# Performance work log

Measured on AMD Instinct MI355X. Metric: run time of the kernel, lower is better.

The kernel has to match this reference:

```python
import jax, jax.numpy as jnp
import numpy as np

B, S, D = 2, 2048, 2048
H, KVH, HD = 16, 8, 128
EPS = 1e-6
ROPE_THETA = 10000.0


def _rope_cache(seq_len, head_dim):
    inv_freq = 1.0 / (ROPE_THETA ** (np.arange(0, head_dim, 2, dtype=np.float32) / head_dim))
    t = np.arange(seq_len, dtype=np.float32)
    freqs = np.outer(t, inv_freq)                      # [S, HD/2]
    emb = np.concatenate([freqs, freqs], axis=-1)      # [S, HD]
    return jnp.asarray(np.cos(emb)), jnp.asarray(np.sin(emb))


def setup_inputs() -> dict:
    key = jax.random.key(0)
    ks = jax.random.split(key, 10)
    x = jax.random.normal(ks[0], (B, S, D), dtype=jnp.float32)
    wq_q = jax.random.randint(ks[1], (H * HD, D), -127, 128, dtype=jnp.int32)
    wk_q = jax.random.randint(ks[2], (KVH * HD, D), -127, 128, dtype=jnp.int32)
    wv_q = jax.random.randint(ks[3], (KVH * HD, D), -127, 128, dtype=jnp.int32)
    wo_q = jax.random.randint(ks[4], (D, H * HD), -127, 128, dtype=jnp.int32)
    # per-output-channel scales (realistic small magnitudes)
    wq_s = jax.random.uniform(ks[5], (H * HD,), minval=1e-3, maxval=2e-2)
    wk_s = jax.random.uniform(ks[6], (KVH * HD,), minval=1e-3, maxval=2e-2)
    wv_s = jax.random.uniform(ks[7], (KVH * HD,), minval=1e-3, maxval=2e-2)
    wo_s = jax.random.uniform(ks[8], (D,), minval=1e-3, maxval=2e-2)
    q_norm_w = jnp.ones((HD,), dtype=jnp.float32)
    k_norm_w = jnp.ones((HD,), dtype=jnp.float32)
    cos_cache, sin_cache = _rope_cache(S, HD)
    return {"x": x, "wq_q": wq_q, "wq_s": wq_s, "wk_q": wk_q, "wk_s": wk_s,
            "wv_q": wv_q, "wv_s": wv_s, "wo_q": wo_q, "wo_s": wo_s,
            "q_norm_w": q_norm_w, "k_norm_w": k_norm_w,
            "cos_cache": cos_cache, "sin_cache": sin_cache}


def _dequant_linear(x, wq, ws):
    # W8A16-style: dequantize int8 weight with per-channel scale, then GEMM
    w = wq.astype(jnp.float32) * ws[:, None]   # [out, in]
    return x @ w.T


def _rms_norm(x, w, eps=EPS):
    var = jnp.mean(x * x, axis=-1, keepdims=True)
    return x * jax.lax.rsqrt(var + eps) * w


def _rotate_half(x):
    x1, x2 = jnp.split(x, 2, axis=-1)
    return jnp.concatenate([-x2, x1], axis=-1)


def _apply_rope(q, k, cos, sin):
    # q: [B,S,H,HD], k: [B,S,KVH,HD]; cos/sin: [S,HD] -> broadcast over batch, heads
    cos = cos[None, :, None, :]
    sin = sin[None, :, None, :]
    q = q * cos + _rotate_half(q) * sin
    k = k * cos + _rotate_half(k) * sin
    return q, k


def reference(x, wq_q, wq_s, wk_q, wk_s, wv_q, wv_s, wo_q, wo_s,
              q_norm_w, k_norm_w, cos_cache, sin_cache):
    batch, seq_len, dim = x.shape
    q = _dequant_linear(x, wq_q, wq_s).reshape(batch, seq_len, H, HD)
    k = _dequant_linear(x, wk_q, wk_s).reshape(batch, seq_len, KVH, HD)
    v = _dequant_linear(x, wv_q, wv_s).reshape(batch, seq_len, KVH, HD)
    q = _rms_norm(q, q_norm_w)
    k = _rms_norm(k, k_norm_w)
    # first forward: cache is empty -> kv = current k,v
    q, k = _apply_rope(q, k, cos_cache[:seq_len], sin_cache[:seq_len])
    q = q.transpose(0, 2, 1, 3)   # [B,H,S,HD]
    k = k.transpose(0, 2, 1, 3)   # [B,KVH,S,HD]
    v = v.transpose(0, 2, 1, 3)
    rep = H // KVH
    k = jnp.repeat(k, rep, axis=1)  # GQA repeat_interleave -> [B,H,S,HD]
    v = jnp.repeat(v, rep, axis=1)
    scale = 1.0 / jnp.sqrt(jnp.asarray(HD, dtype=x.dtype))
    scores = jnp.einsum('bhqd,bhkd->bhqk', q, k) * scale
    causal = jnp.tril(jnp.ones((seq_len, seq_len), dtype=bool))
    scores = jnp.where(causal[None, None], scores, jnp.finfo(scores.dtype).min)
    attn = jax.nn.softmax(scores, axis=-1)
    out = jnp.einsum('bhqk,bhkd->bhqd', attn, v)
    out = out.transpose(0, 2, 1, 3).reshape(batch, seq_len, H * HD)
    return _dequant_linear(out, wo_q, wo_s)
```

## Files before the change

### kernel.cpp

```cpp
#include <hip/hip_runtime.h>


typedef __attribute__((ext_vector_type(4))) float floatx4;
typedef __attribute__((ext_vector_type(8))) short short8v;
typedef __attribute__((ext_vector_type(4))) short short4v;
typedef __attribute__((ext_vector_type(8))) unsigned short ushort8v;
typedef __attribute__((ext_vector_type(4))) unsigned short ushort4v;

#define DEVINL __device__ __forceinline__

constexpr int cB = 2, cS = 2048, cD = 2048, cH = 16, cKVH = 8, cHD = 128;
constexpr int cM = cB * cS;
constexpr int cNqkv = (cH + 2 * cKVH) * cHD;
constexpr float cEPS = 1e-6f;
constexpr float cSCALE = 0.08838834764831845f;

DEVINL unsigned short f2bf(float f) {
  unsigned u = __float_as_uint(f);
  unsigned r = ((u >> 16) & 1u) + 0x7FFFu;
  return (unsigned short)((u + r) >> 16);
}
DEVINL float bf2f(unsigned short h) { return __uint_as_float(((unsigned)h) << 16); }

DEVINL floatx4 mfma_bf16(short8v a, short8v b, floatx4 c) {
  return __builtin_amdgcn_mfma_f32_16x16x32_bf16(a, b, c, 0, 0, 0);
}

DEVINL floatx4 mfma_pv(short4v a, short4v b, floatx4 c) {
#if __has_builtin(__builtin_amdgcn_mfma_f32_16x16x16bf16_1k)
  return __builtin_amdgcn_mfma_f32_16x16x16bf16_1k(a, b, c, 0, 0, 0);
#else
  short8v a8 = {a[0], a[1], a[2], a[3], (short)0, (short)0, (short)0, (short)0};
  short8v b8 = {b[0], b[1], b[2], b[3], (short)0, (short)0, (short)0, (short)0};
  return __builtin_amdgcn_mfma_f32_16x16x32_bf16(a8, b8, c, 0, 0, 0);
#endif
}

DEVINL void gl_lds16(const void* g, void* l) {
  __builtin_amdgcn_global_load_lds(
      (const __attribute__((address_space(1))) void*)g,
      (__attribute__((address_space(3))) void*)l, 16, 0, 0);
}

__global__ void detect_dtype(const unsigned* __restrict__ x, int* __restrict__ flag) {
  __shared__ int cnt;
  if (threadIdx.x == 0) cnt = 0;
  __syncthreads();
  int c = 0;
  for (int i = threadIdx.x; i < 4096; i += 256) {
    unsigned e = (x[i] >> 7) & 0xFFu;
    c += (e >= 100u && e <= 142u) ? 1 : 0;
  }
  atomicAdd(&cnt, c);
  __syncthreads();
  if (threadIdx.x == 0) *flag = (cnt > 2457) ? 1 : 0;
}

__global__ void conv_x(const void* __restrict__ src, unsigned short* __restrict__ dst,
                       int n, const int* __restrict__ flag) {
  int i = (blockIdx.x * 256 + threadIdx.x) * 8;
  if (i >= n) return;
  if (*flag) {
    *(ushort8v*)(dst + i) = *(const ushort8v*)((const unsigned short*)src + i);
  } else {
    const float* s = (const float*)src;
    ushort8v o;
#pragma unroll
    for (int j = 0; j < 8; j++) o[j] = f2bf(s[i + j]);
    *(ushort8v*)(dst + i) = o;
  }
}

__global__ void conv_f32(const void* __restrict__ src, float* __restrict__ dst,
                         int n, const int* __restrict__ flag) {
  int i = blockIdx.x * 256 + threadIdx.x;
  if (i >= n) return;
  dst[i] = (*flag) ? bf2f(((const unsigned short*)src)[i]) : ((const float*)src)[i];
}

__global__ void conv_w(const int* __restrict__ w, unsigned short* __restrict__ dst, int n) {
  int i = (blockIdx.x * 256 + threadIdx.x) * 4;
  if (i >= n) return;
  int4 v = *(const int4*)(w + i);
  ushort4v o;
  o[0] = f2bf((float)v.x); o[1] = f2bf((float)v.y);
  o[2] = f2bf((float)v.z); o[3] = f2bf((float)v.w);
  *(ushort4v*)(dst + i) = o;
}

__global__ void rope_pack(const void* __restrict__ cosc, const void* __restrict__ sinc,
                          float2* __restrict__ tab, const int* __restrict__ flag) {
  int i = blockIdx.x * 256 + threadIdx.x;
  if (i >= cS * 64) return;
  int s = i >> 6, t = i & 63;
  int f = *flag;
  float c = f ? bf2f(((const unsigned short*)cosc)[s * cHD + t])
              : ((const float*)cosc)[s * cHD + t];
  float sn = f ? bf2f(((const unsigned short*)sinc)[s * cHD + t])
               : ((const float*)sinc)[s * cHD + t];
  tab[i] = make_float2(c, sn);
}

__global__ __launch_bounds__(256) void gemm_qkv(
    const unsigned short* __restrict__ A, const unsigned short* __restrict__ Bw,
    const float* __restrict__ colscale, const float2* __restrict__ ropetab,
    const float* __restrict__ nw, unsigned short* __restrict__ Qb,
    unsigned short* __restrict__ Kb, unsigned short* __restrict__ Vt) {
  __shared__ float4 smem4[2192];
  char* smem = (char*)smem4;
  unsigned short* As = (unsigned short*)smem;
  unsigned short* Bs = As + 8192;
  const int tid = threadIdx.x;
  const int lane = tid & 63, wave = tid >> 6;
  const int q = lane >> 4, l16 = lane & 15;
  const int m0 = blockIdx.y * 128, n0 = blockIdx.x * 128;
  const int wm = (wave & 1) * 64, wn = (wave >> 1) * 64;

  floatx4 acc[4][4] = {};

  int goff[4];
#pragma unroll
  for (int i = 0; i < 4; i++) {
    int s = (wave * 4 + i) * 64 + lane;
    int r = s >> 3, u = (s & 7) ^ (r & 7);
    goff[i] = r * cD + u * 8;
  }
  const unsigned short* Ag = A + (size_t)m0 * cD;
  const unsigned short* Bg = Bw + (size_t)n0 * cD;

  for (int k0 = 0; k0 < cD; k0 += 64) {
    __syncthreads();
#pragma unroll
    for (int i = 0; i < 4; i++)
      gl_lds16(Ag + k0 + goff[i], (char*)As + (wave * 4 + i) * 1024);
#pragma unroll
    for (int i = 0; i < 4; i++)
      gl_lds16(Bg + k0 + goff[i], (char*)Bs + (wave * 4 + i) * 1024);
    __syncthreads();
#pragma unroll
    for (int kk = 0; kk < 2; kk++) {
      short8v af[4], bf[4];
#pragma unroll
      for (int mt = 0; mt < 4; mt++) {
        int row = wm + mt * 16 + l16;
        af[mt] = *(const short8v*)(As + row * 64 + (((kk * 4 + q) ^ (l16 & 7)) * 8));
      }
#pragma unroll
      for (int nt = 0; nt < 4; nt++) {
        int row = wn + nt * 16 + l16;
        bf[nt] = *(const short8v*)(Bs + row * 64 + (((kk * 4 + q) ^ (l16 & 7)) * 8));
      }
#pragma unroll
      for (int mt = 0; mt < 4; mt++)
#pragma unroll
        for (int nt = 0; nt < 4; nt++)
          acc[mt][nt] = mfma_bf16(af[mt], bf[nt], acc[mt][nt]);
    }
  }

  float sc[4];
#pragma unroll
  for (int nt = 0; nt < 4; nt++) sc[nt] = colscale[n0 + wn + nt * 16 + l16];
#pragma unroll
  for (int mt = 0; mt < 4; mt++)
#pragma unroll
    for (int nt = 0; nt < 4; nt++)
#pragma unroll
      for (int rg = 0; rg < 4; rg++) acc[mt][nt][rg] *= sc[nt];

  const int tile_n = blockIdx.x;
  const int bi = m0 >> 11, sbase = m0 & (cS - 1);
  __syncthreads();

  if (tile_n >= 24) {
    unsigned short* T = (unsigned short*)smem;
#pragma unroll
    for (int mt = 0; mt < 4; mt++)
#pragma unroll
      for (int nt = 0; nt < 4; nt++) {
        short4v pk;
#pragma unroll
        for (int rg = 0; rg < 4; rg++) pk[rg] = (short)f2bf(acc[mt][nt][rg]);
        *(short4v*)(T + (wn + nt * 16 + l16) * 136 + (wm + mt * 16 + q * 4)) = pk;
      }
    __syncthreads();
    const int d = tid >> 1, sh = (tid & 1) * 64;
    unsigned short* dst = Vt + ((size_t)(bi * cKVH + (tile_n - 24)) * cHD + d) * cS
                          + sbase + sh;
#pragma unroll
    for (int j = 0; j < 8; j++)
      *(ushort8v*)(dst + j * 8) = *(const ushort8v*)(T + d * 136 + sh + j * 8);
  } else {
    unsigned short* W = (unsigned short*)smem;
    float* ssq  = (float*)(smem + 32768);
    float* invs = (float*)(smem + 33792);

    float sl[4][4];
#pragma unroll
    for (int mt = 0; mt < 4; mt++)
#pragma unroll
      for (int rg = 0; rg < 4; rg++) {
        float s = 0.f;
#pragma unroll
        for (int nt = 0; nt < 4; nt++) s += acc[mt][nt][rg] * acc[mt][nt][rg];
        s += __shfl_xor(s, 1); s += __shfl_xor(s, 2);
        s += __shfl_xor(s, 4); s += __shfl_xor(s, 8);
        sl[mt][rg] = s;
      }
    unsigned short* Wo = W + wave * 4096;
#pragma unroll
    for (int mt = 0; mt < 4; mt++)
#pragma unroll
      for (int nt = 0; nt < 4; nt++) {
        short4v pk;
#pragma unroll
        for (int rg = 0; rg < 4; rg++) pk[rg] = (short)f2bf(acc[mt][nt][rg]);
        *(short4v*)(Wo + (mt * 4 + nt) * 256 + lane * 4) = pk;
      }
    if (l16 == 0) {
#pragma unroll
      for (int mt = 0; mt < 4; mt++)
#pragma unroll
        for (int rg = 0; rg < 4; rg++)
          ssq[((wave >> 1) & 1) * 128 + wm + mt * 16 + q * 4 + rg] = sl[mt][rg];
    }
    __syncthreads();
    if (tid < 128)
      invs[tid] = rsqrtf((ssq[tid] + ssq[128 + tid]) * (1.0f / cHD) + cEPS);
    __syncthreads();

    const unsigned short* Wp = W + (wave ^ 2) * 4096;
    const int wn1 = wave >> 1;
    const float* nwb = nw + (tile_n < 16 ? 0 : cHD);
    float wown[4], wpar[4];
#pragma unroll
    for (int nt = 0; nt < 4; nt++) {
      wown[nt] = nwb[wn1 * 64 + nt * 16 + l16];
      wpar[nt] = nwb[(wn1 ^ 1) * 64 + nt * 16 + l16];
    }
    unsigned short* dstb = (tile_n < 16)
        ? Qb + ((size_t)(bi * cH + tile_n) * cS) * cHD
        : Kb + ((size_t)(bi * cKVH + (tile_n - 16)) * cS) * cHD;
#pragma unroll
    for (int mt = 0; mt < 4; mt++) {
      float iv[4];
#pragma unroll
      for (int rg = 0; rg < 4; rg++) iv[rg] = invs[wm + mt * 16 + q * 4 + rg];
#pragma unroll
      for (int nt = 0; nt < 4; nt++) {
        short4v pk = *(const short4v*)(Wp + (mt * 4 + nt) * 256 + lane * 4);
#pragma unroll
        for (int rg = 0; rg < 4; rg++) {
          int srow = sbase + wm + mt * 16 + q * 4 + rg;
          float2 cs = ropetab[srow * 64 + nt * 16 + l16];
          float nown = acc[mt][nt][rg] * iv[rg] * wown[nt];
          float npar = bf2f((unsigned short)pk[rg]) * iv[rg] * wpar[nt];
          float o = wn1 == 0 ? nown * cs.x - npar * cs.y
                             : nown * cs.x + npar * cs.y;
          dstb[(size_t)srow * cHD + wn1 * 64 + nt * 16 + l16] = f2bf(o);
        }
      }
    }
  }
}

__global__ __launch_bounds__(256) void gemm_out(
    const unsigned short* __restrict__ A, const unsigned short* __restrict__ Bw,
    const float* __restrict__ colscale, void* __restrict__ Cout,
    const int* __restrict__ flag, int M, int N, int K) {
  __shared__ unsigned short As[128 * 64];
  __shared__ unsigned short Bs[128 * 64];
  const int tid = threadIdx.x;
  const int lane = tid & 63, wave = tid >> 6;
  const int q = lane >> 4, l16 = lane & 15;
  const int m0 = blockIdx.y * 128, n0 = blockIdx.x * 128;
  const int wm = (wave & 1) * 64, wn = (wave >> 1) * 64;

  floatx4 acc[4][4] = {};

  int goff[4];
#pragma unroll
  for (int i = 0; i < 4; i++) {
    int s = (wave * 4 + i) * 64 + lane;
    int r = s >> 3, u = (s & 7) ^ (r & 7);
    goff[i] = r * K + u * 8;
  }
  const unsigned short* Ag = A + (size_t)m0 * K;
  const unsigned short* Bg = Bw + (size_t)n0 * K;

  for (int k0 = 0; k0 < K; k0 += 64) {
    __syncthreads();
#pragma unroll
    for (int i = 0; i < 4; i++)
      gl_lds16(Ag + k0 + goff[i], (char*)As + (wave * 4 + i) * 1024);
#pragma unroll
    for (int i = 0; i < 4; i++)
      gl_lds16(Bg + k0 + goff[i], (char*)Bs + (wave * 4 + i) * 1024);
    __syncthreads();
#pragma unroll
    for (int kk = 0; kk < 2; kk++) {
      short8v af[4], bf[4];
#pragma unroll
      for (int mt = 0; mt < 4; mt++) {
        int row = wm + mt * 16 + l16;
        af[mt] = *(const short8v*)(As + row * 64 + (((kk * 4 + q) ^ (l16 & 7)) * 8));
      }
#pragma unroll
      for (int nt = 0; nt < 4; nt++) {
        int row = wn + nt * 16 + l16;
        bf[nt] = *(const short8v*)(Bs + row * 64 + (((kk * 4 + q) ^ (l16 & 7)) * 8));
      }
#pragma unroll
      for (int mt = 0; mt < 4; mt++)
#pragma unroll
        for (int nt = 0; nt < 4; nt++)
          acc[mt][nt] = mfma_bf16(af[mt], bf[nt], acc[mt][nt]);
    }
  }
  const int f = *flag;
#pragma unroll
  for (int mt = 0; mt < 4; mt++) {
    int r0 = m0 + wm + mt * 16 + q * 4;
#pragma unroll
    for (int nt = 0; nt < 4; nt++) {
      int cn = n0 + wn + nt * 16 + l16;
      float sc = colscale[cn];
#pragma unroll
      for (int rg = 0; rg < 4; rg++) {
        float v = acc[mt][nt][rg] * sc;
        if (f) ((unsigned short*)Cout)[(size_t)(r0 + rg) * N + cn] = f2bf(v);
        else   ((float*)Cout)[(size_t)(r0 + rg) * N + cn] = v;
      }
    }
  }
}

__global__ __launch_bounds__(256, 2) void attn(
    const unsigned short* __restrict__ Qb, const unsigned short* __restrict__ Kb,
    const unsigned short* __restrict__ Vt, unsigned short* __restrict__ AO) {
  __shared__ unsigned short SM[32768];
  const int tid = threadIdx.x;
  const int lane = tid & 63, wv = tid >> 6;
  const int q = lane >> 4, l16 = lane & 15;
  const int bi = blockIdx.z, h = blockIdx.y;
  const int kh = h >> 1;
  const int qt = (int)gridDim.x - 1 - (int)blockIdx.x;
  const int q0 = qt * 64;
  const int q0w = q0 + wv * 16;

  const unsigned short* Qbase = Qb + ((size_t)(bi * cH + h) * cS + q0w) * cHD;
  const unsigned short* Kbase = Kb + ((size_t)(bi * cKVH + kh) * cS) * cHD;
  const unsigned short* Vbase = Vt + ((size_t)(bi * cKVH + kh) * cHD) * cS;

  short8v qa[4];
#pragma unroll
  for (int c = 0; c < 4; c++)
    qa[c] = *(const short8v*)(Qbase + (size_t)l16 * cHD + c * 32 + q * 8);

  floatx4 oacc[8] = {};
  float lp = 0.f;

  int koff[4], voff[4];
#pragma unroll
  for (int i = 0; i < 4; i++) {
    int s = (wv * 4 + i) * 64 + lane;
    int r = s >> 4, u = (s & 15) ^ (r & 15);
    koff[i] = r * cHD + u * 8;
    int d = s >> 3, uv = (s & 7) ^ (d & 7);
    voff[i] = d * cS + uv * 8;
  }

  auto stage = [&](int win) {
    const int buf = (win & 1) * 16384;
    const int kv0 = win * 64;
    unsigned short* Kdst = SM + buf + (wv * 4) * 512;
    unsigned short* Vdst = SM + buf + 8192 + (wv * 4) * 512;
#pragma unroll
    for (int i = 0; i < 4; i++)
      gl_lds16(Kbase + (size_t)kv0 * cHD + koff[i], Kdst + i * 512);
#pragma unroll
    for (int i = 0; i < 4; i++)
      gl_lds16(Vbase + (size_t)kv0 + voff[i], Vdst + i * 512);
  };

  stage(0);
  for (int win = 0; win <= qt; win++) {
    __syncthreads();
    if (win < qt) stage(win + 1);
    const unsigned short* Ks = SM + (win & 1) * 16384;
    const unsigned short* Vs = Ks + 8192;

    floatx4 sres[4] = {};
#pragma unroll
    for (int c = 0; c < 4; c++) {
      short8v kf[4];
#pragma unroll
      for (int ntk = 0; ntk < 4; ntk++)
        kf[ntk] = *(const short8v*)(Ks + (ntk * 16 + l16) * 128 + (((c * 4 + q) ^ l16) * 8));
#pragma unroll
      for (int ntk = 0; ntk < 4; ntk++)
        sres[ntk] = mfma_bf16(kf[ntk], qa[c], sres[ntk]);
    }

    const bool lastwin = (win == qt);
    short4v pa[4];
#pragma unroll
    for (int ntk = 0; ntk < 4; ntk++) {
#pragma unroll
      for (int rg = 0; rg < 4; rg++) {
        float e = __expf(sres[ntk][rg] * cSCALE);
        if (lastwin && (ntk * 16 + q * 4 + rg > wv * 16 + l16)) e = 0.f;
        lp += e;
        pa[ntk][rg] = (short)f2bf(e);
      }
    }

#pragma unroll
    for (int ntk = 0; ntk < 4; ntk++) {
#pragma unroll
      for (int db = 0; db < 8; db++) {
        short4v vb = *(const short4v*)(Vs + (db * 16 + l16) * 64 +
                       (((ntk * 2 + (q >> 1)) ^ (l16 & 7)) * 8 + (q & 1) * 4));
        oacc[db] = mfma_pv(pa[ntk], vb, oacc[db]);
      }
    }
  }

  float lf = lp;
  lf += __shfl_xor(lf, 16);
  lf += __shfl_xor(lf, 32);
  float li[4];
#pragma unroll
  for (int rg = 0; rg < 4; rg++) li[rg] = 1.0f / __shfl(lf, q * 4 + rg);

#pragma unroll
  for (int rg = 0; rg < 4; rg++) {
    int row = q0w + q * 4 + rg;
    unsigned short* dst = AO + (size_t)(bi * cS + row) * (cH * cHD) + h * cHD;
#pragma unroll
    for (int db = 0; db < 8; db++)
      dst[db * 16 + l16] = f2bf(oacc[db][rg] * li[rg]);
  }
}

extern "C" void kernel_launch(void* const* d_in, const int* in_sizes, int n_in,
                              void* d_out, int out_size, void* d_ws, size_t ws_size,
                              hipStream_t stream) {
  (void)in_sizes; (void)n_in; (void)out_size; (void)ws_size;
  char* ws = (char*)d_ws;
  size_t off = 0;
  auto alloc = [&](size_t bytes) -> char* {
    char* p = ws + off;
    off += (bytes + 255) & ~((size_t)255);
    return p;
  };
  int* flag            = (int*)alloc(256);
  float2* ropetab      = (float2*)alloc((size_t)cS * 64 * 8);
  float* nw            = (float*)alloc(256 * 4);
  float* scat          = (float*)alloc(4096 * 4);
  float* so            = (float*)alloc(2048 * 4);
  unsigned short* xb   = (unsigned short*)alloc((size_t)cM * cD * 2);
  unsigned short* wcat = (unsigned short*)alloc((size_t)cNqkv * cD * 2);
  unsigned short* wob  = (unsigned short*)alloc((size_t)cD * cH * cHD * 2);
  unsigned short* Qb   = (unsigned short*)alloc((size_t)cB * cH * cS * cHD * 2);
  unsigned short* Kb   = (unsigned short*)alloc((size_t)cB * cKVH * cS * cHD * 2);
  unsigned short* Vt   = (unsigned short*)alloc((size_t)cB * cKVH * cHD * cS * 2);
  unsigned short* AO   = (unsigned short*)alloc((size_t)cM * cD * 2);

  detect_dtype<<<1, 256, 0, stream>>>((const unsigned*)d_in[0], flag);

  conv_x<<<(cM * cD / 8 + 255) / 256, 256, 0, stream>>>(d_in[0], xb, cM * cD, flag);
  rope_pack<<<(cS * 64 + 255) / 256, 256, 0, stream>>>(d_in[11], d_in[12], ropetab, flag);
  conv_f32<<<1, 256, 0, stream>>>(d_in[9], nw, cHD, flag);
  conv_f32<<<1, 256, 0, stream>>>(d_in[10], nw + cHD, cHD, flag);
  conv_f32<<<8, 256, 0, stream>>>(d_in[2], scat, 2048, flag);
  conv_f32<<<4, 256, 0, stream>>>(d_in[4], scat + 2048, 1024, flag);
  conv_f32<<<4, 256, 0, stream>>>(d_in[6], scat + 3072, 1024, flag);
  conv_f32<<<8, 256, 0, stream>>>(d_in[8], so, 2048, flag);
  conv_w<<<(2048 * 2048 / 4 + 255) / 256, 256, 0, stream>>>((const int*)d_in[1], wcat, 2048 * 2048);
  conv_w<<<(1024 * 2048 / 4 + 255) / 256, 256, 0, stream>>>((const int*)d_in[3], wcat + (size_t)2048 * 2048, 1024 * 2048);
  conv_w<<<(1024 * 2048 / 4 + 255) / 256, 256, 0, stream>>>((const int*)d_in[5], wcat + (size_t)3072 * 2048, 1024 * 2048);
  conv_w<<<(2048 * 2048 / 4 + 255) / 256, 256, 0, stream>>>((const int*)d_in[7], wob, 2048 * 2048);

  gemm_qkv<<<dim3(cNqkv / 128, cM / 128), 256, 0, stream>>>(
      xb, wcat, scat, ropetab, nw, Qb, Kb, Vt);
  attn<<<dim3(cS / 64, cH, cB), 256, 0, stream>>>(Qb, Kb, Vt, AO);
  gemm_out<<<dim3(cD / 128, cM / 128), 256, 0, stream>>>(
      AO, wob, so, d_out, flag, cM, cD, cH * cHD);
}
```

Before: 476.3 us.

## Pre-pack GEMM operands into MFMA fragment order and load directly to registers

Replaces the row-major bf16 conversion kernels with a pack_frag kernel that writes activations and weights in MFMA fragment-major layout. Both GEMMs then read fragments straight from global memory into registers with a two-stage register double buffer, so the LDS staging and per-iteration barriers go away. The cost is an extra pack pass over the attention output before the output projection, plus an extra workspace buffer. Register-direct loads also give up LDS reuse across waves, so each wave refetches its A and B fragments from cache.

```diff
diff --git a/kernel.cpp b/kernel.cpp
--- a/kernel.cpp
+++ b/kernel.cpp
@@ -5,7 +5,6 @@
 typedef __attribute__((ext_vector_type(8))) short short8v;
 typedef __attribute__((ext_vector_type(4))) short short4v;
 typedef __attribute__((ext_vector_type(8))) unsigned short ushort8v;
-typedef __attribute__((ext_vector_type(4))) unsigned short ushort4v;
 
 #define DEVINL __device__ __forceinline__
 
@@ -56,18 +55,35 @@
   if (threadIdx.x == 0) *flag = (cnt > 2457) ? 1 : 0;
 }
 
-__global__ void conv_x(const void* __restrict__ src, unsigned short* __restrict__ dst,
-                       int n, const int* __restrict__ flag) {
-  int i = (blockIdx.x * 256 + threadIdx.x) * 8;
-  if (i >= n) return;
-  if (*flag) {
-    *(ushort8v*)(dst + i) = *(const ushort8v*)((const unsigned short*)src + i);
-  } else {
-    const float* s = (const float*)src;
+__global__ __launch_bounds__(256) void pack_frag(
+    const void* __restrict__ src, unsigned short* __restrict__ dst,
+    int K, int mode, const int* __restrict__ flag) {
+  __shared__ float L[16][264];
+  const int T = blockIdx.x, kc = blockIdx.y;
+  const int tid = threadIdx.x;
+  int md = mode;
+  if (md == 0) md = (*flag) ? 3 : 1;
+#pragma unroll
+  for (int it = 0; it < 16; it++) {
+    int e = it * 256 + tid;
+    int r = e >> 8, c = e & 255;
+    size_t idx = (size_t)(T * 16 + r) * K + kc * 256 + c;
+    float v;
+    if (md == 1)      v = ((const float*)src)[idx];
+    else if (md == 2) v = (float)((const int*)src)[idx];
+    else              v = bf2f(((const unsigned short*)src)[idx]);
+    L[r][c] = v;
+  }
+  __syncthreads();
+  const int lane = tid & 63, w = tid >> 6;
+  const int q = lane >> 4, l16 = lane & 15;
+#pragma unroll
+  for (int p = 0; p < 2; p++) {
+    int kbl = w + p * 4;
     ushort8v o;
 #pragma unroll
-    for (int j = 0; j < 8; j++) o[j] = f2bf(s[i + j]);
-    *(ushort8v*)(dst + i) = o;
+    for (int j = 0; j < 8; j++) o[j] = f2bf(L[l16][kbl * 32 + q * 8 + j]);
+    *(ushort8v*)(dst + ((size_t)T * 64 + kc * 8 + kbl) * 512 + lane * 8) = o;
   }
 }
 
@@ -76,16 +92,6 @@
   int i = blockIdx.x * 256 + threadIdx.x;
   if (i >= n) return;
   dst[i] = (*flag) ? bf2f(((const unsigned short*)src)[i]) : ((const float*)src)[i];
-}
-
-__global__ void conv_w(const int* __restrict__ w, unsigned short* __restrict__ dst, int n) {
-  int i = (blockIdx.x * 256 + threadIdx.x) * 4;
-  if (i >= n) return;
-  int4 v = *(const int4*)(w + i);
-  ushort4v o;
-  o[0] = f2bf((float)v.x); o[1] = f2bf((float)v.y);
-  o[2] = f2bf((float)v.z); o[3] = f2bf((float)v.w);
-  *(ushort4v*)(dst + i) = o;
 }
 
 __global__ void rope_pack(const void* __restrict__ cosc, const void* __restrict__ sinc,
@@ -101,15 +107,58 @@
   tab[i] = make_float2(c, sn);
 }
 
+DEVINL void gemm_core_rr(const unsigned short* __restrict__ Ap,
+                         const unsigned short* __restrict__ Bp,
+                         int tm0, int tn0, int nkb, int lane,
+                         floatx4 acc[4][4]) {
+  const unsigned short* ap[4];
+  const unsigned short* bp[4];
+#pragma unroll
+  for (int i = 0; i < 4; i++) {
+    ap[i] = Ap + ((size_t)(tm0 + i) * 64) * 512 + lane * 8;
+    bp[i] = Bp + ((size_t)(tn0 + i) * 64) * 512 + lane * 8;
+  }
+  short8v a0[4], b0[4], a1[4], b1[4];
+#pragma unroll
+  for (int i = 0; i < 4; i++) {
+    a0[i] = *(const short8v*)(ap[i]);
+    b0[i] = *(const short8v*)(bp[i]);
+  }
+  for (int kb = 0; kb < nkb; kb += 2) {
+    const int o1 = (kb + 1) * 512;
+#pragma unroll
+    for (int i = 0; i < 4; i++) {
+      a1[i] = *(const short8v*)(ap[i] + o1);
+      b1[i] = *(const short8v*)(bp[i] + o1);
+    }
+#pragma unroll
+    for (int mt = 0; mt < 4; mt++)
+#pragma unroll
+      for (int nt = 0; nt < 4; nt++)
+        acc[mt][nt] = mfma_bf16(a0[mt], b0[nt], acc[mt][nt]);
+    if (kb + 2 < nkb) {
+      const int o2 = (kb + 2) * 512;
+#pragma unroll
+      for (int i = 0; i < 4; i++) {
+        a0[i] = *(const short8v*)(ap[i] + o2);
+        b0[i] = *(const short8v*)(bp[i] + o2);
+      }
+    }
+#pragma unroll
+    for (int mt = 0; mt < 4; mt++)
+#pragma unroll
+      for (int nt = 0; nt < 4; nt++)
+        acc[mt][nt] = mfma_bf16(a1[mt], b1[nt], acc[mt][nt]);
+  }
+}
+
 __global__ __launch_bounds__(256) void gemm_qkv(
-    const unsigned short* __restrict__ A, const unsigned short* __restrict__ Bw,
+    const unsigned short* __restrict__ Ap, const unsigned short* __restrict__ Bp,
     const float* __restrict__ colscale, const float2* __restrict__ ropetab,
     const float* __restrict__ nw, unsigned short* __restrict__ Qb,
     unsigned short* __restrict__ Kb, unsigned short* __restrict__ Vt) {
   __shared__ float4 smem4[2192];
   char* smem = (char*)smem4;
-  unsigned short* As = (unsigned short*)smem;
-  unsigned short* Bs = As + 8192;
   const int tid = threadIdx.x;
   const int lane = tid & 63, wave = tid >> 6;
   const int q = lane >> 4, l16 = lane & 15;
@@ -117,46 +166,7 @@
   const int wm = (wave & 1) * 64, wn = (wave >> 1) * 64;
 
   floatx4 acc[4][4] = {};
-
-  int goff[4];
-#pragma unroll
-  for (int i = 0; i < 4; i++) {
-    int s = (wave * 4 + i) * 64 + lane;
-    int r = s >> 3, u = (s & 7) ^ (r & 7);
-    goff[i] = r * cD + u * 8;
-  }
-  const unsigned short* Ag = A + (size_t)m0 * cD;
-  const unsigned short* Bg = Bw + (size_t)n0 * cD;
-
-  for (int k0 = 0; k0 < cD; k0 += 64) {
-    __syncthreads();
-#pragma unroll
-    for (int i = 0; i < 4; i++)
-      gl_lds16(Ag + k0 + goff[i], (char*)As + (wave * 4 + i) * 1024);
-#pragma unroll
-    for (int i = 0; i < 4; i++)
-      gl_lds16(Bg + k0 + goff[i], (char*)Bs + (wave * 4 + i) * 1024);
-    __syncthreads();
-#pragma unroll
-    for (int kk = 0; kk < 2; kk++) {
-      short8v af[4], bf[4];
-#pragma unroll
-      for (int mt = 0; mt < 4; mt++) {
-        int row = wm + mt * 16 + l16;
-        af[mt] = *(const short8v*)(As + row * 64 + (((kk * 4 + q) ^ (l16 & 7)) * 8));
-      }
-#pragma unroll
-      for (int nt = 0; nt < 4; nt++) {
-        int row = wn + nt * 16 + l16;
-        bf[nt] = *(const short8v*)(Bs + row * 64 + (((kk * 4 + q) ^ (l16 & 7)) * 8));
-      }
-#pragma unroll
-      for (int mt = 0; mt < 4; mt++)
-#pragma unroll
-        for (int nt = 0; nt < 4; nt++)
-          acc[mt][nt] = mfma_bf16(af[mt], bf[nt], acc[mt][nt]);
-    }
-  }
+  gemm_core_rr(Ap, Bp, (m0 + wm) >> 4, (n0 + wn) >> 4, cD / 32, lane, acc);
 
   float sc[4];
 #pragma unroll
@@ -170,7 +180,6 @@
 
   const int tile_n = blockIdx.x;
   const int bi = m0 >> 11, sbase = m0 & (cS - 1);
-  __syncthreads();
 
   if (tile_n >= 24) {
     unsigned short* T = (unsigned short*)smem;
@@ -265,11 +274,9 @@
 }
 
 __global__ __launch_bounds__(256) void gemm_out(
-    const unsigned short* __restrict__ A, const unsigned short* __restrict__ Bw,
+    const unsigned short* __restrict__ Ap, const unsigned short* __restrict__ Bp,
     const float* __restrict__ colscale, void* __restrict__ Cout,
-    const int* __restrict__ flag, int M, int N, int K) {
-  __shared__ unsigned short As[128 * 64];
-  __shared__ unsigned short Bs[128 * 64];
+    const int* __restrict__ flag, int N, int nkb) {
   const int tid = threadIdx.x;
   const int lane = tid & 63, wave = tid >> 6;
   const int q = lane >> 4, l16 = lane & 15;
@@ -277,46 +284,8 @@
   const int wm = (wave & 1) * 64, wn = (wave >> 1) * 64;
 
   floatx4 acc[4][4] = {};
-
-  int goff[4];
-#pragma unroll
-  for (int i = 0; i < 4; i++) {
-    int s = (wave * 4 + i) * 64 + lane;
-    int r = s >> 3, u = (s & 7) ^ (r & 7);
-    goff[i] = r * K + u * 8;
-  }
-  const unsigned short* Ag = A + (size_t)m0 * K;
-  const unsigned short* Bg = Bw + (size_t)n0 * K;
-
-  for (int k0 = 0; k0 < K; k0 += 64) {
-    __syncthreads();
-#pragma unroll
-    for (int i = 0; i < 4; i++)
-      gl_lds16(Ag + k0 + goff[i], (char*)As + (wave * 4 + i) * 1024);
-#pragma unroll
-    for (int i = 0; i < 4; i++)
-      gl_lds16(Bg + k0 + goff[i], (char*)Bs + (wave * 4 + i) * 1024);
-    __syncthreads();
-#pragma unroll
-    for (int kk = 0; kk < 2; kk++) {
-      short8v af[4], bf[4];
-#pragma unroll
-      for (int mt = 0; mt < 4; mt++) {
-        int row = wm + mt * 16 + l16;
-        af[mt] = *(const short8v*)(As + row * 64 + (((kk * 4 + q) ^ (l16 & 7)) * 8));
-      }
-#pragma unroll
-      for (int nt = 0; nt < 4; nt++) {
-        int row = wn + nt * 16 + l16;
-        bf[nt] = *(const short8v*)(Bs + row * 64 + (((kk * 4 + q) ^ (l16 & 7)) * 8));
-      }
-#pragma unroll
-      for (int mt = 0; mt < 4; mt++)
-#pragma unroll
-        for (int nt = 0; nt < 4; nt++)
-          acc[mt][nt] = mfma_bf16(af[mt], bf[nt], acc[mt][nt]);
-    }
-  }
+  gemm_core_rr(Ap, Bp, (m0 + wm) >> 4, (n0 + wn) >> 4, nkb, lane, acc);
+
   const int f = *flag;
 #pragma unroll
   for (int mt = 0; mt < 4; mt++) {
@@ -459,17 +428,23 @@
   float* nw            = (float*)alloc(256 * 4);
   float* scat          = (float*)alloc(4096 * 4);
   float* so            = (float*)alloc(2048 * 4);
-  unsigned short* xb   = (unsigned short*)alloc((size_t)cM * cD * 2);
-  unsigned short* wcat = (unsigned short*)alloc((size_t)cNqkv * cD * 2);
-  unsigned short* wob  = (unsigned short*)alloc((size_t)cD * cH * cHD * 2);
+  unsigned short* xp   = (unsigned short*)alloc((size_t)cM * cD * 2);
+  unsigned short* wp   = (unsigned short*)alloc((size_t)cNqkv * cD * 2);
+  unsigned short* wop  = (unsigned short*)alloc((size_t)cD * cH * cHD * 2);
   unsigned short* Qb   = (unsigned short*)alloc((size_t)cB * cH * cS * cHD * 2);
   unsigned short* Kb   = (unsigned short*)alloc((size_t)cB * cKVH * cS * cHD * 2);
   unsigned short* Vt   = (unsigned short*)alloc((size_t)cB * cKVH * cHD * cS * 2);
   unsigned short* AO   = (unsigned short*)alloc((size_t)cM * cD * 2);
+  unsigned short* AOp  = (unsigned short*)alloc((size_t)cM * cD * 2);
 
   detect_dtype<<<1, 256, 0, stream>>>((const unsigned*)d_in[0], flag);
 
-  conv_x<<<(cM * cD / 8 + 255) / 256, 256, 0, stream>>>(d_in[0], xb, cM * cD, flag);
+  pack_frag<<<dim3(256, 8), 256, 0, stream>>>(d_in[0], xp, 2048, 0, flag);
+  pack_frag<<<dim3(128, 8), 256, 0, stream>>>(d_in[1], wp, 2048, 2, flag);
+  pack_frag<<<dim3(64, 8), 256, 0, stream>>>(d_in[3], wp + (size_t)128 * 64 * 512, 2048, 2, flag);
+  pack_frag<<<dim3(64, 8), 256, 0, stream>>>(d_in[5], wp + (size_t)192 * 64 * 512, 2048, 2, flag);
+  pack_frag<<<dim3(128, 8), 256, 0, stream>>>(d_in[7], wop, 2048, 2, flag);
+
   rope_pack<<<(cS * 64 + 255) / 256, 256, 0, stream>>>(d_in[11], d_in[12], ropetab, flag);
   conv_f32<<<1, 256, 0, stream>>>(d_in[9], nw, cHD, flag);
   conv_f32<<<1, 256, 0, stream>>>(d_in[10], nw + cHD, cHD, flag);
@@ -477,14 +452,11 @@
   conv_f32<<<4, 256, 0, stream>>>(d_in[4], scat + 2048, 1024, flag);
   conv_f32<<<4, 256, 0, stream>>>(d_in[6], scat + 3072, 1024, flag);
   conv_f32<<<8, 256, 0, stream>>>(d_in[8], so, 2048, flag);
-  conv_w<<<(2048 * 2048 / 4 + 255) / 256, 256, 0, stream>>>((const int*)d_in[1], wcat, 2048 * 2048);
-  conv_w<<<(1024 * 2048 / 4 + 255) / 256, 256, 0, stream>>>((const int*)d_in[3], wcat + (size_t)2048 * 2048, 1024 * 2048);
-  conv_w<<<(1024 * 2048 / 4 + 255) / 256, 256, 0, stream>>>((const int*)d_in[5], wcat + (size_t)3072 * 2048, 1024 * 2048);
-  conv_w<<<(2048 * 2048 / 4 + 255) / 256, 256, 0, stream>>>((const int*)d_in[7], wob, 2048 * 2048);
 
   gemm_qkv<<<dim3(cNqkv / 128, cM / 128), 256, 0, stream>>>(
-      xb, wcat, scat, ropetab, nw, Qb, Kb, Vt);
+      xp, wp, scat, ropetab, nw, Qb, Kb, Vt);
   attn<<<dim3(cS / 64, cH, cB), 256, 0, stream>>>(Qb, Kb, Vt, AO);
+  pack_frag<<<dim3(256, 8), 256, 0, stream>>>(AO, AOp, 2048, 3, flag);
   gemm_out<<<dim3(cD / 128, cM / 128), 256, 0, stream>>>(
-      AO, wob, so, d_out, flag, cM, cD, cH * cHD);
-}
+      AOp, wop, so, d_out, flag, cD, (cH * cHD) / 32);
+}
```

Measured after the change: 497.8 us. 4.5% more time.
